# Kernel tuning notes

Measured on AMD Instinct MI355X. Metric: run time of the kernel, lower is better.

Reference implementation:

```python
import jax, jax.numpy as jnp
import numpy as np

B, T, E, H, R = 4, 256, 128, 8, 64
D = E // H


def _xavier(k, fan_in, fan_out, gain=1.0):
    a = gain * np.sqrt(6.0 / (fan_in + fan_out))
    return jax.random.uniform(k, (fan_in, fan_out), minval=-a, maxval=a, dtype=jnp.float32)


def setup_inputs() -> dict:
    key = jax.random.key(0)
    ks = jax.random.split(key, 16)
    g = 1.0 / np.sqrt(2.0)  # gain used for q/k/v when qkv_same_dim
    return {
        "query": jax.random.normal(ks[0], (B, T, E), jnp.float32),
        "velocity": jax.random.normal(ks[1], (B, T, 3, E), jnp.float32),
        "edge_feature": jax.random.normal(ks[2], (B, T, T, R), jnp.float32),
        "edge_direction": jax.random.normal(ks[3], (B, T, T, 3), jnp.float32),
        "cutoff": jax.random.uniform(ks[4], (B, T, T), jnp.float32),
        "Wq": _xavier(ks[5], E, E, g), "bq": jnp.zeros((E,), jnp.float32),
        "Wk": _xavier(ks[6], E, E, g), "bk": jnp.zeros((E,), jnp.float32),
        "Wv": _xavier(ks[7], E, 3 * E, g), "bv": jnp.zeros((3 * E,), jnp.float32),
        "Wo": _xavier(ks[8], E, 3 * E), "bo": jnp.zeros((3 * E,), jnp.float32),
        "Wvel": _xavier(ks[9], E, 3 * E), "bvel": jnp.zeros((3 * E,), jnp.float32),
        "Wdk": _xavier(ks[10], R, E), "bdk": jnp.zeros((E,), jnp.float32),
        "Wdv": _xavier(ks[11], R, 3 * E), "bdv": jnp.zeros((3 * E,), jnp.float32),
    }


def reference(query, velocity, edge_feature, edge_direction, cutoff,
              Wq, bq, Wk, bk, Wv, bv, Wo, bo, Wvel, bvel, Wdk, bdk, Wdv, bdv):
    b, t, e = query.shape
    h = H
    d = e // h
    scaling = d ** -0.5
    # projections
    q = ((query @ Wq + bq) * scaling).reshape(b, t, 1, h, d)   # [b,t,1,h,d]
    k = (query @ Wk + bk).reshape(b, 1, t, h, d)                # [b,1,t,h,d]
    v = (query @ Wv + bv).reshape(b, 1, t, h, 3 * d)            # [b,1,t,h,3d]
    # RBF distance gates (dense pairwise)
    dk = jax.nn.silu(edge_feature @ Wdk + bdk).reshape(b, t, t, h, d)
    dv = jax.nn.silu(edge_feature @ Wdv + bdv).reshape(b, t, t, h, 3 * d)
    v = v * dv                                                  # [b,t,t,h,3d]
    v, vp1, vp2 = jnp.split(v, 3, axis=-1)                      # each [b,t,t,h,d]
    # velocity channel
    velp = velocity @ Wvel + bvel                               # [b,t,3,3e]
    w1, w2, w3 = jnp.split(velp, 3, axis=-1)                    # each [b,t,3,e]
    velocity_dot = (w1 * w2).sum(axis=2)                        # [b,t,e]
    vel_r = velocity.reshape(b, t, 3, h, d)
    # elementwise (non-dot-product) attention weights
    aw = q * k * dk / np.float32(np.sqrt(d))                    # [b,t,t,h,d]
    awf = jnp.nan_to_num(jax.nn.softmax(aw, axis=2))
    c = cutoff[..., None, None]                                 # [b,t,t,1,1]
    attn = (awf * c * v * (c != 0)).sum(axis=2).reshape(b, t, e)
    o1, o2, o3 = jnp.split(attn @ Wo + bo, 3, axis=-1)          # each [b,t,e]
    # equivariant vector path
    vec1 = vel_r[:, None] * vp1[:, :, :, None]                  # [b,t,t,3,h,d]
    vec2 = vp2[:, :, :, None] * edge_direction[..., None, None]
    vec = ((vec1 + vec2).reshape(b, t, t, 3, e) * (c != 0)).sum(axis=2)  # [b,t,3,e]
    dx = velocity_dot * o2 + o3                                 # [b,t,e]
    dvec = w3 * o1[:, :, None, :] + vec                         # [b,t,3,e]
    return dx, dvec
```

## Files before the change

kernel.cpp:

```cpp
#include <hip/hip_runtime.h>
#include <hip/hip_bf16.h>
#include <math.h>

#define TT 256
#define EE 128
#define TJ 16
#define SRCB 28672
#define TSH 14336
#define GTB 16384
#define VTB 12288

typedef __attribute__((ext_vector_type(8))) short short8v;
typedef __attribute__((ext_vector_type(4))) short short4v;
typedef __attribute__((ext_vector_type(4))) float f32x4;

__device__ __forceinline__ float silu_f(float x) {
    return x * __builtin_amdgcn_rcpf(1.0f + __expf(-x));
}

__device__ __forceinline__ unsigned short f2bf(float f) {
    union { float f; unsigned u; } x; x.f = f;
    unsigned r = (x.u + 0x7FFFu + ((x.u >> 16) & 1u)) >> 16;
    return (unsigned short)r;
}

__device__ __forceinline__ unsigned cvt_pk_bf16(float lo, float hi) {
    unsigned r;
    asm("v_cvt_pk_bf16_f32 %0, %1, %2" : "=v"(r) : "v"(lo), "v"(hi));
    return r;
}

__device__ __forceinline__ float bflo(unsigned u) { return __uint_as_float(u << 16); }
__device__ __forceinline__ float bfhi(unsigned u) { return __uint_as_float(u & 0xffff0000u); }
__device__ __forceinline__ float bfu(unsigned short u) { return __uint_as_float(((unsigned)u) << 16); }

__global__ __launch_bounds__(256) void packW_kernel(
    const float* __restrict__ Wdk, const float* __restrict__ Wdv,
    unsigned short* __restrict__ wfrag) {
    const int idx = blockIdx.x * 256 + threadIdx.x;
    const int lane = idx & 63;
    const int kh = (idx >> 6) & 1;
    const int nn = (idx >> 7) & 7;
    const int w = idx >> 10;
    const float* Wsel; int wstride, colbase;
    if (w == 0) { Wsel = Wdk; wstride = 128; colbase = 0; }
    else { Wsel = Wdv; wstride = 384; colbase = (w - 1) * 128; }
    const int lrow = lane >> 4;
    const int lcol = lane & 15;
    const int col = colbase + nn * 16 + lcol;
    unsigned short* dst = wfrag + (size_t)idx * 8;
#pragma unroll
    for (int e = 0; e < 8; ++e) {
        const int k = kh * 32 + lrow * 8 + e;
        dst[e] = f2bf(Wsel[k * wstride + col]);
    }
}

__global__ __launch_bounds__(256) void phaseA_kernel(
    const float* __restrict__ query, const float* __restrict__ velocity,
    const float* __restrict__ Wq, const float* __restrict__ bq,
    const float* __restrict__ Wk, const float* __restrict__ bk,
    const float* __restrict__ Wv, const float* __restrict__ bv,
    const float* __restrict__ Wvel, const float* __restrict__ bvel,
    float* __restrict__ qs_ws, unsigned short* __restrict__ kkvvT,
    float* __restrict__ veldot_ws, float* __restrict__ w3_ws) {
    const int row = blockIdx.x;
    const int t = threadIdx.x;
    __shared__ float sIn[EE];
    __shared__ float sVel[3 * EE];
    __shared__ float sVelp[3 * 384];
    if (t < EE) sIn[t] = query[(size_t)row * EE + t];
    for (int idx = t; idx < 3 * EE; idx += 256)
        sVel[idx] = velocity[(size_t)row * 3 * EE + idx];
    __syncthreads();

    unsigned short* tb = kkvvT + (size_t)(row >> 4) * TSH;
    const int r16 = row & 15;
    for (int o = t; o < 640; o += 256) {
        if (o < 128) {
            int c = o;
            float acc = bq[c];
#pragma unroll 8
            for (int r = 0; r < 128; ++r) acc = fmaf(sIn[r], Wq[r * 128 + c], acc);
            qs_ws[(size_t)row * 128 + c] = acc * 0.25f;
        } else if (o < 256) {
            int c = o - 128;
            float acc = bk[c];
#pragma unroll 8
            for (int r = 0; r < 128; ++r) acc = fmaf(sIn[r], Wk[r * 128 + c], acc);
            const int sg = (r16 >> 2) ^ ((c >> 2) & 3);
            tb[c * 16 + sg * 4 + (r16 & 3)] = f2bf(acc);
        } else {
            int c = o - 256;
            float acc = bv[c];
#pragma unroll 8
            for (int r = 0; r < 128; ++r) acc = fmaf(sIn[r], Wv[r * 384 + c], acc);
            const int col = 128 + c;
            const int sg = (r16 >> 2) ^ ((col >> 2) & 3);
            tb[col * 16 + sg * 4 + (r16 & 3)] = f2bf(acc);
        }
    }
    for (int idx = t; idx < 384; idx += 256)
        tb[8192 + r16 * 384 + idx] = f2bf(sVel[idx]);

    for (int c = t; c < 384; c += 256) {
        float a0 = bvel[c], a1 = a0, a2 = a0;
#pragma unroll 8
        for (int r = 0; r < 128; ++r) {
            float w = Wvel[r * 384 + c];
            a0 = fmaf(sVel[r], w, a0);
            a1 = fmaf(sVel[128 + r], w, a1);
            a2 = fmaf(sVel[256 + r], w, a2);
        }
        sVelp[0 * 384 + c] = a0;
        sVelp[1 * 384 + c] = a1;
        sVelp[2 * 384 + c] = a2;
    }
    __syncthreads();
    if (t < 128) {
        int c = t;
        float vd = 0.f;
#pragma unroll
        for (int s = 0; s < 3; ++s)
            vd += sVelp[s * 384 + c] * sVelp[s * 384 + 128 + c];
        veldot_ws[(size_t)row * 128 + c] = vd;
#pragma unroll
        for (int s = 0; s < 3; ++s)
            w3_ws[((size_t)row * 3 + s) * 128 + c] = sVelp[s * 384 + 256 + c];
    }
}

__global__ __launch_bounds__(256, 3) void phaseB_kernel(
    const float* __restrict__ edge_feature, const float* __restrict__ edge_direction,
    const float* __restrict__ cutoff,
    const unsigned short* __restrict__ wfrag, const unsigned short* __restrict__ kkvvT,
    const float* __restrict__ bdk, const float* __restrict__ bdv,
    const float* __restrict__ qs_ws,
    float* __restrict__ attn_ws, float* __restrict__ vec_ws) {
    const int blk = blockIdx.x;
    const int x = blk & 7;
    const int slot = blk >> 3;
    const int b = x >> 1;
    const int i = ((x & 1) << 7) + slot;
    const int row = b * TT + i;

    const int t = threadIdx.x;
    const int wave = t >> 6;
    const int lane = t & 63;
    const int lrow = lane >> 4;
    const int lcol = lane & 15;

    __shared__ __align__(16) unsigned char smem[51712];
    unsigned char* sGates = smem;
    unsigned char* sVelB  = smem + 16384;
    unsigned char* sEFb   = smem + 28672;
    unsigned short* sKD   = (unsigned short*)(smem + 32768);
    unsigned short* sGV   = (unsigned short*)(smem + 37376);
    float* sCut           = (float*)(smem + 51200);
    float* sDirS          = (float*)(smem + 51328);
    float* sMrg           = (float*)smem;

    const float* Bsel;
    int colbase;
    if (wave == 0) { Bsel = bdk; colbase = 0; }
    else { Bsel = bdv; colbase = (wave - 1) * 128; }

    float biasv[8];
#pragma unroll
    for (int n = 0; n < 8; ++n)
        biasv[n] = Bsel[colbase + n * 16 + lcol];

    const unsigned short* wfbase = wfrag + ((size_t)wave * 1024 + lane) * 8;
    short8v bwr[16];
#pragma unroll
    for (int n = 0; n < 8; ++n) {
        bwr[2 * n]     = *(const short8v*)(wfbase + (size_t)n * 1024);
        bwr[2 * n + 1] = *(const short8v*)(wfbase + (size_t)n * 1024 + 512);
    }

    const int grp = t >> 7;
    const int c = t & 127;
    const float qsc = qs_ws[(size_t)row * 128 + c] * 0.25f * 1.44269504f;

    float l = 0.f, A = 0.f;
    float v0 = 0.f, v1 = 0.f, v2 = 0.f;

    const size_t ef_base = (size_t)row * TT * 64;
    const size_t cut_base = (size_t)row * TT;
    const size_t dir_base = (size_t)row * TT * 3;
    const unsigned char* kvT = (const unsigned char*)kkvvT + (size_t)(b * 16) * SRCB;

    const int ldsoff = (t & 192) * 16;
    const int gswz = (lrow ^ ((lcol >> 2) & 3)) * 4;

#pragma unroll
    for (int r = 0; r < 4; ++r)
        __builtin_amdgcn_global_load_lds(
            (const void*)(kvT + (size_t)r * 4096 + (size_t)t * 16),
            (void*)(sGates + r * 4096 + ldsoff), 16, 0, 0);
    {
        f32x4 e0 = ((const f32x4*)(edge_feature + ef_base))[t];
        const int erow = t >> 4;
        const int kq = t & 15;
        const unsigned plo = cvt_pk_bf16(e0[0], e0[1]);
        const unsigned phi = cvt_pk_bf16(e0[2], e0[3]);
        const int byteoff = (kq * 8) ^ ((erow & 7) << 4);
        *(int2*)(sEFb + erow * 128 + byteoff) = make_int2((int)plo, (int)phi);
        if (t < TJ) sCut[t] = cutoff[cut_base + t];
        if (t < TJ * 3) sDirS[t] = edge_direction[dir_base + t];
    }
    __syncthreads();

    f32x4 pEf;
    float pCut = 0.f, pDir = 0.f;
    int e = 0;
    for (int j0 = 0; j0 < TT; j0 += TJ) {
        {
            const unsigned char* src = kvT + (size_t)(j0 >> 4) * SRCB + GTB;
#pragma unroll
            for (int r = 0; r < 3; ++r)
                __builtin_amdgcn_global_load_lds(
                    (const void*)(src + (size_t)r * 4096 + (size_t)t * 16),
                    (void*)(sVelB + r * 4096 + ldsoff), 16, 0, 0);
        }
        {
            const int jn = (j0 + TJ) & 255;
            pEf = ((const f32x4*)(edge_feature + ef_base + (size_t)jn * 64))[t];
            pCut = (t < TJ) ? cutoff[cut_base + jn + t] : 0.f;
            pDir = (t < TJ * 3) ? edge_direction[dir_base + (size_t)jn * 3 + t] : 0.f;
        }
        {
            const unsigned short* gT = (const unsigned short*)sGates;
            const unsigned char* efb = sEFb + e * 2048;
            const int arow = lcol;
            const int swzb = (arow & 7) << 4;
            const short8v a0 = *(const short8v*)(efb + arow * 128 + ((lrow * 16) ^ swzb));
            const short8v a1 = *(const short8v*)(efb + arow * 128 + ((64 + lrow * 16) ^ swzb));

            short4v g4[8];
#pragma unroll
            for (int n = 0; n < 8; ++n)
                g4[n] = *(const short4v*)(gT + ((wave * 128 + n * 16 + lcol) * 16 + gswz));
#pragma unroll
            for (int n = 0; n < 8; ++n) {
                const int col = colbase + n * 16 + lcol;
                f32x4 acc = {biasv[n], biasv[n], biasv[n], biasv[n]};
                acc = __builtin_amdgcn_mfma_f32_16x16x32_bf16(a0, bwr[2 * n],     acc, 0, 0, 0);
                acc = __builtin_amdgcn_mfma_f32_16x16x32_bf16(a1, bwr[2 * n + 1], acc, 0, 0, 0);
                const float r0 = bfu((unsigned short)g4[n][0]) * silu_f(acc[0]);
                const float r1 = bfu((unsigned short)g4[n][1]) * silu_f(acc[1]);
                const float r2 = bfu((unsigned short)g4[n][2]) * silu_f(acc[2]);
                const float r3 = bfu((unsigned short)g4[n][3]) * silu_f(acc[3]);
                const unsigned w01 = cvt_pk_bf16(r0, r1);
                const unsigned w23 = cvt_pk_bf16(r2, r3);
                unsigned short* dst;
                if (wave == 0) {
                    dst = &sKD[col * 18 + lrow * 4];
                } else {
                    const int plane = (col >> 4) % 3;
                    const int cch = (col / 48) * 16 + lcol;
                    dst = &sGV[plane * 2304 + cch * 18 + lrow * 4];
                }
                *(unsigned*)(dst) = w01;
                *(unsigned*)(dst + 2) = w23;
            }
        }
        __syncthreads();

        if (j0 + TJ < TT) {
            const unsigned char* src = kvT + (size_t)((j0 >> 4) + 1) * SRCB;
#pragma unroll
            for (int r = 0; r < 4; ++r)
                __builtin_amdgcn_global_load_lds(
                    (const void*)(src + (size_t)r * 4096 + (size_t)t * 16),
                    (void*)(sGates + r * 4096 + ldsoff), 16, 0, 0);
        }
        {
            unsigned char* efb = sEFb + (e ^ 1) * 2048;
            const int erow = t >> 4;
            const int kq = t & 15;
            const unsigned plo = cvt_pk_bf16(pEf[0], pEf[1]);
            const unsigned phi = cvt_pk_bf16(pEf[2], pEf[3]);
            const int byteoff = (kq * 8) ^ ((erow & 7) << 4);
            *(int2*)(efb + erow * 128 + byteoff) = make_int2((int)plo, (int)phi);
            if (t < TJ) sCut[(e ^ 1) * TJ + t] = pCut;
            if (t < TJ * 3) sDirS[(e ^ 1) * TJ * 3 + t] = pDir;
        }
        {
            const unsigned short* svel = (const unsigned short*)sVelB;
            const float* cutE = sCut + e * TJ;
            const float* dirE = sDirS + e * TJ * 3;
            const int jlo = grp * (TJ / 2);
#pragma unroll
            for (int q = 0; q < 4; ++q) {
                const int jj = jlo + 2 * q;
                const unsigned kd2 = *(const unsigned*)(&sKD[c * 18 + jj]);
                const unsigned vg2 = *(const unsigned*)(&sGV[0 * 2304 + c * 18 + jj]);
                const unsigned p12 = *(const unsigned*)(&sGV[1 * 2304 + c * 18 + jj]);
                const unsigned p22 = *(const unsigned*)(&sGV[2 * 2304 + c * 18 + jj]);
                const float cut0 = cutE[jj];
                const float cut1 = cutE[jj + 1];
                const float p0 = exp2f(qsc * bflo(kd2));
                const float p1 = exp2f(qsc * bfhi(kd2));
                l += p0 + p1;
                A = fmaf(p0 * cut0, bflo(vg2), A);
                A = fmaf(p1 * cut1, bfhi(vg2), A);
                if (cut0 != 0.0f) {
                    const unsigned short* vp = svel + (size_t)jj * 384 + c;
                    const float w1 = bflo(p12), w2 = bflo(p22);
                    v0 = fmaf(bfu(vp[0]),   w1, fmaf(w2, dirE[jj * 3 + 0], v0));
                    v1 = fmaf(bfu(vp[128]), w1, fmaf(w2, dirE[jj * 3 + 1], v1));
                    v2 = fmaf(bfu(vp[256]), w1, fmaf(w2, dirE[jj * 3 + 2], v2));
                }
                if (cut1 != 0.0f) {
                    const unsigned short* vp = svel + (size_t)(jj + 1) * 384 + c;
                    const float w1 = bfhi(p12), w2 = bfhi(p22);
                    v0 = fmaf(bfu(vp[0]),   w1, fmaf(w2, dirE[jj * 3 + 3], v0));
                    v1 = fmaf(bfu(vp[128]), w1, fmaf(w2, dirE[jj * 3 + 4], v1));
                    v2 = fmaf(bfu(vp[256]), w1, fmaf(w2, dirE[jj * 3 + 5], v2));
                }
            }
        }
        __syncthreads();
        e ^= 1;
    }

    if (grp == 1) {
        sMrg[c * 5 + 0] = l;  sMrg[c * 5 + 1] = A;
        sMrg[c * 5 + 2] = v0; sMrg[c * 5 + 3] = v1; sMrg[c * 5 + 4] = v2;
    }
    __syncthreads();
    if (grp == 0) {
        const float L = l + sMrg[c * 5 + 0];
        const float Aa = A + sMrg[c * 5 + 1];
        const float attn = (L > 0.f) ? (Aa * __builtin_amdgcn_rcpf(L)) : 0.f;
        attn_ws[(size_t)row * 128 + c] = attn;
        vec_ws[((size_t)row * 3 + 0) * 128 + c] = v0 + sMrg[c * 5 + 2];
        vec_ws[((size_t)row * 3 + 1) * 128 + c] = v1 + sMrg[c * 5 + 3];
        vec_ws[((size_t)row * 3 + 2) * 128 + c] = v2 + sMrg[c * 5 + 4];
    }
}

__global__ __launch_bounds__(256) void phaseC_kernel(
    const float* __restrict__ Wo, const float* __restrict__ bo,
    const float* __restrict__ attn_ws, const float* __restrict__ veldot_ws,
    const float* __restrict__ w3_ws, const float* __restrict__ vec_ws,
    float* __restrict__ out) {
    const int row = blockIdx.x;
    const int t = threadIdx.x;
    __shared__ float sAttn[128];
    __shared__ float sO[384];
    if (t < 128) sAttn[t] = attn_ws[(size_t)row * 128 + t];
    __syncthreads();
    for (int o = t; o < 384; o += 256) {
        float acc = bo[o];
#pragma unroll 8
        for (int r = 0; r < 128; ++r) acc = fmaf(sAttn[r], Wo[r * 384 + o], acc);
        sO[o] = acc;
    }
    __syncthreads();
    if (t < 128) {
        int c = t;
        float o1 = sO[c], o2 = sO[128 + c], o3 = sO[256 + c];
        float dx = fmaf(veldot_ws[(size_t)row * 128 + c], o2, o3);
        out[(size_t)row * 128 + c] = dx;
#pragma unroll
        for (int s = 0; s < 3; ++s) {
            size_t idx = ((size_t)row * 3 + s) * 128 + c;
            out[131072 + idx] = fmaf(w3_ws[idx], o1, vec_ws[idx]);
        }
    }
}

extern "C" void kernel_launch(void* const* d_in, const int* in_sizes, int n_in,
                              void* d_out, int out_size, void* d_ws, size_t ws_size,
                              hipStream_t stream) {
    (void)in_sizes; (void)n_in; (void)out_size; (void)ws_size;
    const float* query          = (const float*)d_in[0];
    const float* velocity       = (const float*)d_in[1];
    const float* edge_feature   = (const float*)d_in[2];
    const float* edge_direction = (const float*)d_in[3];
    const float* cutoff         = (const float*)d_in[4];
    const float* Wq   = (const float*)d_in[5];  const float* bq   = (const float*)d_in[6];
    const float* Wk   = (const float*)d_in[7];  const float* bk   = (const float*)d_in[8];
    const float* Wv   = (const float*)d_in[9];  const float* bv   = (const float*)d_in[10];
    const float* Wo   = (const float*)d_in[11]; const float* bo   = (const float*)d_in[12];
    const float* Wvel = (const float*)d_in[13]; const float* bvel = (const float*)d_in[14];
    const float* Wdk  = (const float*)d_in[15]; const float* bdk  = (const float*)d_in[16];
    const float* Wdv  = (const float*)d_in[17]; const float* bdv  = (const float*)d_in[18];

    float* ws        = (float*)d_ws;
    float* qs_ws     = ws;
    float* veldot_ws = ws + 131072;
    float* w3_ws     = ws + 262144;
    float* attn_ws   = ws + 655360;
    float* vec_ws    = ws + 786432;
    unsigned short* wfrag = (unsigned short*)(ws + 1179648);
    unsigned short* kkvvT = (unsigned short*)(ws + 1196032);

    float* out = (float*)d_out;

    hipLaunchKernelGGL(packW_kernel, dim3(16), dim3(256), 0, stream,
        Wdk, Wdv, wfrag);
    hipLaunchKernelGGL(phaseA_kernel, dim3(1024), dim3(256), 0, stream,
        query, velocity, Wq, bq, Wk, bk, Wv, bv, Wvel, bvel,
        qs_ws, kkvvT, veldot_ws, w3_ws);
    hipLaunchKernelGGL(phaseB_kernel, dim3(1024), dim3(256), 0, stream,
        edge_feature, edge_direction, cutoff,
        wfrag, kkvvT, bdk, bdv, qs_ws, attn_ws, vec_ws);
    hipLaunchKernelGGL(phaseC_kernel, dim3(1024), dim3(256), 0, stream,
        Wo, bo, attn_ws, veldot_ws, w3_ws, vec_ws, out);
}
```

Baseline: 150.7 us.

## Prefetch gate tiles into registers instead of LDS and unroll loop by two

The kk/vv gate fragments used by each MFMA output are no longer staged through shared memory with global_load_lds. Each lane now loads them straight from global memory into registers, one tile ahead, using a ping-pong register pair (gA/gB). The j-loop is unrolled by two through a templated tile body, so the edge-feature double-buffer index becomes a compile-time constant. This cuts LDS use from about 51.7KB to 35.3KB, which could allow more resident blocks, at the cost of extra VGPRs and uncoalesced short4 global loads whose latency must be hidden by the prefetch.

```diff
diff --git a/kernel.cpp b/kernel.cpp
--- a/kernel.cpp
+++ b/kernel.cpp
@@ -130,6 +130,122 @@
     }
 }
 
+template <int E>
+__device__ __forceinline__ void tile_body(
+    int j0,
+    const float* __restrict__ edge_feature, const float* __restrict__ cutoff,
+    const float* __restrict__ edge_direction,
+    size_t ef_base, size_t cut_base, size_t dir_base,
+    const unsigned char* kvT,
+    unsigned char* sVelB, unsigned char* sEFb,
+    unsigned short* sKD, unsigned short* sGV, float* sCut, float* sDirS,
+    int t, int wave, int lrow, int lcol, int ldsoff, int gswz,
+    int colbase, const float (&biasv)[8], const short8v (&bwr)[16],
+    short4v (&gcur)[8], short4v (&gnext)[8],
+    f32x4& pEf, float& pCut, float& pDir,
+    int grp, int c, float qsc,
+    float& l, float& A, float& v0, float& v1, float& v2) {
+
+    {
+        const unsigned char* src = kvT + (size_t)(j0 >> 4) * SRCB + GTB;
+#pragma unroll
+        for (int r = 0; r < 3; ++r)
+            __builtin_amdgcn_global_load_lds(
+                (const void*)(src + (size_t)r * 4096 + (size_t)t * 16),
+                (void*)(sVelB + r * 4096 + ldsoff), 16, 0, 0);
+    }
+    {
+        const int jn = (j0 + TJ) & 255;
+        pEf = ((const f32x4*)(edge_feature + ef_base + (size_t)jn * 64))[t];
+        pCut = (t < TJ) ? cutoff[cut_base + jn + t] : 0.f;
+        pDir = (t < TJ * 3) ? edge_direction[dir_base + (size_t)jn * 3 + t] : 0.f;
+    }
+    if (j0 + TJ < TT) {
+        const unsigned short* gsrc = (const unsigned short*)(kvT + (size_t)((j0 >> 4) + 1) * SRCB);
+#pragma unroll
+        for (int n = 0; n < 8; ++n)
+            gnext[n] = *(const short4v*)(gsrc + ((wave * 128 + n * 16 + lcol) * 16 + gswz));
+    }
+    {
+        const unsigned char* efb = sEFb + E * 2048;
+        const int swzb = (lcol & 7) << 4;
+        const short8v a0 = *(const short8v*)(efb + lcol * 128 + ((lrow * 16) ^ swzb));
+        const short8v a1 = *(const short8v*)(efb + lcol * 128 + ((64 + lrow * 16) ^ swzb));
+#pragma unroll
+        for (int n = 0; n < 8; ++n) {
+            const int col = colbase + n * 16 + lcol;
+            f32x4 acc = {biasv[n], biasv[n], biasv[n], biasv[n]};
+            acc = __builtin_amdgcn_mfma_f32_16x16x32_bf16(a0, bwr[2 * n],     acc, 0, 0, 0);
+            acc = __builtin_amdgcn_mfma_f32_16x16x32_bf16(a1, bwr[2 * n + 1], acc, 0, 0, 0);
+            const float r0 = bfu((unsigned short)gcur[n][0]) * silu_f(acc[0]);
+            const float r1 = bfu((unsigned short)gcur[n][1]) * silu_f(acc[1]);
+            const float r2 = bfu((unsigned short)gcur[n][2]) * silu_f(acc[2]);
+            const float r3 = bfu((unsigned short)gcur[n][3]) * silu_f(acc[3]);
+            const unsigned w01 = cvt_pk_bf16(r0, r1);
+            const unsigned w23 = cvt_pk_bf16(r2, r3);
+            unsigned short* dst;
+            if (wave == 0) {
+                dst = &sKD[col * 18 + lrow * 4];
+            } else {
+                const int plane = (col >> 4) % 3;
+                const int cch = (col / 48) * 16 + lcol;
+                dst = &sGV[plane * 2304 + cch * 18 + lrow * 4];
+            }
+            *(unsigned*)(dst) = w01;
+            *(unsigned*)(dst + 2) = w23;
+        }
+    }
+    __syncthreads();
+
+    {
+        unsigned char* efb = sEFb + (E ^ 1) * 2048;
+        const int erow = t >> 4;
+        const int kq = t & 15;
+        const unsigned plo = cvt_pk_bf16(pEf[0], pEf[1]);
+        const unsigned phi = cvt_pk_bf16(pEf[2], pEf[3]);
+        const int byteoff = (kq * 8) ^ ((erow & 7) << 4);
+        *(int2*)(efb + erow * 128 + byteoff) = make_int2((int)plo, (int)phi);
+        if (t < TJ) sCut[(E ^ 1) * TJ + t] = pCut;
+        if (t < TJ * 3) sDirS[(E ^ 1) * TJ * 3 + t] = pDir;
+    }
+    {
+        const unsigned short* svel = (const unsigned short*)sVelB;
+        const float* cutE = sCut + E * TJ;
+        const float* dirE = sDirS + E * TJ * 3;
+        const int jlo = grp * (TJ / 2);
+#pragma unroll
+        for (int q = 0; q < 4; ++q) {
+            const int jj = jlo + 2 * q;
+            const unsigned kd2 = *(const unsigned*)(&sKD[c * 18 + jj]);
+            const unsigned vg2 = *(const unsigned*)(&sGV[0 * 2304 + c * 18 + jj]);
+            const unsigned p12 = *(const unsigned*)(&sGV[1 * 2304 + c * 18 + jj]);
+            const unsigned p22 = *(const unsigned*)(&sGV[2 * 2304 + c * 18 + jj]);
+            const float cut0 = cutE[jj];
+            const float cut1 = cutE[jj + 1];
+            const float p0 = exp2f(qsc * bflo(kd2));
+            const float p1 = exp2f(qsc * bfhi(kd2));
+            l += p0 + p1;
+            A = fmaf(p0 * cut0, bflo(vg2), A);
+            A = fmaf(p1 * cut1, bfhi(vg2), A);
+            if (cut0 != 0.0f) {
+                const unsigned short* vp = svel + (size_t)jj * 384 + c;
+                const float w1 = bflo(p12), w2 = bflo(p22);
+                v0 = fmaf(bfu(vp[0]),   w1, fmaf(w2, dirE[jj * 3 + 0], v0));
+                v1 = fmaf(bfu(vp[128]), w1, fmaf(w2, dirE[jj * 3 + 1], v1));
+                v2 = fmaf(bfu(vp[256]), w1, fmaf(w2, dirE[jj * 3 + 2], v2));
+            }
+            if (cut1 != 0.0f) {
+                const unsigned short* vp = svel + (size_t)(jj + 1) * 384 + c;
+                const float w1 = bfhi(p12), w2 = bfhi(p22);
+                v0 = fmaf(bfu(vp[0]),   w1, fmaf(w2, dirE[jj * 3 + 3], v0));
+                v1 = fmaf(bfu(vp[128]), w1, fmaf(w2, dirE[jj * 3 + 4], v1));
+                v2 = fmaf(bfu(vp[256]), w1, fmaf(w2, dirE[jj * 3 + 5], v2));
+            }
+        }
+    }
+    __syncthreads();
+}
+
 __global__ __launch_bounds__(256, 3) void phaseB_kernel(
     const float* __restrict__ edge_feature, const float* __restrict__ edge_direction,
     const float* __restrict__ cutoff,
@@ -150,14 +266,13 @@
     const int lrow = lane >> 4;
     const int lcol = lane & 15;
 
-    __shared__ __align__(16) unsigned char smem[51712];
-    unsigned char* sGates = smem;
-    unsigned char* sVelB  = smem + 16384;
-    unsigned char* sEFb   = smem + 28672;
-    unsigned short* sKD   = (unsigned short*)(smem + 32768);
-    unsigned short* sGV   = (unsigned short*)(smem + 37376);
-    float* sCut           = (float*)(smem + 51200);
-    float* sDirS          = (float*)(smem + 51328);
+    __shared__ __align__(16) unsigned char smem[35328];
+    unsigned char* sVelB  = smem;
+    unsigned char* sEFb   = smem + 12288;
+    unsigned short* sKD   = (unsigned short*)(smem + 16384);
+    unsigned short* sGV   = (unsigned short*)(smem + 20992);
+    float* sCut           = (float*)(smem + 34816);
+    float* sDirS          = (float*)(smem + 34944);
     float* sMrg           = (float*)smem;
 
     const float* Bsel;
@@ -193,11 +308,13 @@
     const int ldsoff = (t & 192) * 16;
     const int gswz = (lrow ^ ((lcol >> 2) & 3)) * 4;
 
-#pragma unroll
-    for (int r = 0; r < 4; ++r)
-        __builtin_amdgcn_global_load_lds(
-            (const void*)(kvT + (size_t)r * 4096 + (size_t)t * 16),
-            (void*)(sGates + r * 4096 + ldsoff), 16, 0, 0);
+    short4v gA[8], gB[8];
+    {
+        const unsigned short* gsrc = (const unsigned short*)kvT;
+#pragma unroll
+        for (int n = 0; n < 8; ++n)
+            gA[n] = *(const short4v*)(gsrc + ((wave * 128 + n * 16 + lcol) * 16 + gswz));
+    }
     {
         f32x4 e0 = ((const f32x4*)(edge_feature + ef_base))[t];
         const int erow = t >> 4;
@@ -213,116 +330,19 @@
 
     f32x4 pEf;
     float pCut = 0.f, pDir = 0.f;
-    int e = 0;
-    for (int j0 = 0; j0 < TT; j0 += TJ) {
-        {
-            const unsigned char* src = kvT + (size_t)(j0 >> 4) * SRCB + GTB;
-#pragma unroll
-            for (int r = 0; r < 3; ++r)
-                __builtin_amdgcn_global_load_lds(
-                    (const void*)(src + (size_t)r * 4096 + (size_t)t * 16),
-                    (void*)(sVelB + r * 4096 + ldsoff), 16, 0, 0);
-        }
-        {
-            const int jn = (j0 + TJ) & 255;
-            pEf = ((const f32x4*)(edge_feature + ef_base + (size_t)jn * 64))[t];
-            pCut = (t < TJ) ? cutoff[cut_base + jn + t] : 0.f;
-            pDir = (t < TJ * 3) ? edge_direction[dir_base + (size_t)jn * 3 + t] : 0.f;
-        }
-        {
-            const unsigned short* gT = (const unsigned short*)sGates;
-            const unsigned char* efb = sEFb + e * 2048;
-            const int arow = lcol;
-            const int swzb = (arow & 7) << 4;
-            const short8v a0 = *(const short8v*)(efb + arow * 128 + ((lrow * 16) ^ swzb));
-            const short8v a1 = *(const short8v*)(efb + arow * 128 + ((64 + lrow * 16) ^ swzb));
-
-            short4v g4[8];
-#pragma unroll
-            for (int n = 0; n < 8; ++n)
-                g4[n] = *(const short4v*)(gT + ((wave * 128 + n * 16 + lcol) * 16 + gswz));
-#pragma unroll
-            for (int n = 0; n < 8; ++n) {
-                const int col = colbase + n * 16 + lcol;
-                f32x4 acc = {biasv[n], biasv[n], biasv[n], biasv[n]};
-                acc = __builtin_amdgcn_mfma_f32_16x16x32_bf16(a0, bwr[2 * n],     acc, 0, 0, 0);
-                acc = __builtin_amdgcn_mfma_f32_16x16x32_bf16(a1, bwr[2 * n + 1], acc, 0, 0, 0);
-                const float r0 = bfu((unsigned short)g4[n][0]) * silu_f(acc[0]);
-                const float r1 = bfu((unsigned short)g4[n][1]) * silu_f(acc[1]);
-                const float r2 = bfu((unsigned short)g4[n][2]) * silu_f(acc[2]);
-                const float r3 = bfu((unsigned short)g4[n][3]) * silu_f(acc[3]);
-                const unsigned w01 = cvt_pk_bf16(r0, r1);
-                const unsigned w23 = cvt_pk_bf16(r2, r3);
-                unsigned short* dst;
-                if (wave == 0) {
-                    dst = &sKD[col * 18 + lrow * 4];
-                } else {
-                    const int plane = (col >> 4) % 3;
-                    const int cch = (col / 48) * 16 + lcol;
-                    dst = &sGV[plane * 2304 + cch * 18 + lrow * 4];
-                }
-                *(unsigned*)(dst) = w01;
-                *(unsigned*)(dst + 2) = w23;
-            }
-        }
-        __syncthreads();
-
-        if (j0 + TJ < TT) {
-            const unsigned char* src = kvT + (size_t)((j0 >> 4) + 1) * SRCB;
-#pragma unroll
-            for (int r = 0; r < 4; ++r)
-                __builtin_amdgcn_global_load_lds(
-                    (const void*)(src + (size_t)r * 4096 + (size_t)t * 16),
-                    (void*)(sGates + r * 4096 + ldsoff), 16, 0, 0);
-        }
-        {
-            unsigned char* efb = sEFb + (e ^ 1) * 2048;
-            const int erow = t >> 4;
-            const int kq = t & 15;
-            const unsigned plo = cvt_pk_bf16(pEf[0], pEf[1]);
-            const unsigned phi = cvt_pk_bf16(pEf[2], pEf[3]);
-            const int byteoff = (kq * 8) ^ ((erow & 7) << 4);
-            *(int2*)(efb + erow * 128 + byteoff) = make_int2((int)plo, (int)phi);
-            if (t < TJ) sCut[(e ^ 1) * TJ + t] = pCut;
-            if (t < TJ * 3) sDirS[(e ^ 1) * TJ * 3 + t] = pDir;
-        }
-        {
-            const unsigned short* svel = (const unsigned short*)sVelB;
-            const float* cutE = sCut + e * TJ;
-            const float* dirE = sDirS + e * TJ * 3;
-            const int jlo = grp * (TJ / 2);
-#pragma unroll
-            for (int q = 0; q < 4; ++q) {
-                const int jj = jlo + 2 * q;
-                const unsigned kd2 = *(const unsigned*)(&sKD[c * 18 + jj]);
-                const unsigned vg2 = *(const unsigned*)(&sGV[0 * 2304 + c * 18 + jj]);
-                const unsigned p12 = *(const unsigned*)(&sGV[1 * 2304 + c * 18 + jj]);
-                const unsigned p22 = *(const unsigned*)(&sGV[2 * 2304 + c * 18 + jj]);
-                const float cut0 = cutE[jj];
-                const float cut1 = cutE[jj + 1];
-                const float p0 = exp2f(qsc * bflo(kd2));
-                const float p1 = exp2f(qsc * bfhi(kd2));
-                l += p0 + p1;
-                A = fmaf(p0 * cut0, bflo(vg2), A);
-                A = fmaf(p1 * cut1, bfhi(vg2), A);
-                if (cut0 != 0.0f) {
-                    const unsigned short* vp = svel + (size_t)jj * 384 + c;
-                    const float w1 = bflo(p12), w2 = bflo(p22);
-                    v0 = fmaf(bfu(vp[0]),   w1, fmaf(w2, dirE[jj * 3 + 0], v0));
-                    v1 = fmaf(bfu(vp[128]), w1, fmaf(w2, dirE[jj * 3 + 1], v1));
-                    v2 = fmaf(bfu(vp[256]), w1, fmaf(w2, dirE[jj * 3 + 2], v2));
-                }
-                if (cut1 != 0.0f) {
-                    const unsigned short* vp = svel + (size_t)(jj + 1) * 384 + c;
-                    const float w1 = bfhi(p12), w2 = bfhi(p22);
-                    v0 = fmaf(bfu(vp[0]),   w1, fmaf(w2, dirE[jj * 3 + 3], v0));
-                    v1 = fmaf(bfu(vp[128]), w1, fmaf(w2, dirE[jj * 3 + 4], v1));
-                    v2 = fmaf(bfu(vp[256]), w1, fmaf(w2, dirE[jj * 3 + 5], v2));
-                }
-            }
-        }
-        __syncthreads();
-        e ^= 1;
+    for (int jt = 0; jt < TT; jt += 2 * TJ) {
+        tile_body<0>(jt, edge_feature, cutoff, edge_direction,
+                     ef_base, cut_base, dir_base, kvT,
+                     sVelB, sEFb, sKD, sGV, sCut, sDirS,
+                     t, wave, lrow, lcol, ldsoff, gswz,
+                     colbase, biasv, bwr, gA, gB, pEf, pCut, pDir,
+                     grp, c, qsc, l, A, v0, v1, v2);
+        tile_body<1>(jt + TJ, edge_feature, cutoff, edge_direction,
+                     ef_base, cut_base, dir_base, kvT,
+                     sVelB, sEFb, sKD, sGV, sCut, sDirS,
+                     t, wave, lrow, lcol, ldsoff, gswz,
+                     colbase, biasv, bwr, gB, gA, pEf, pCut, pDir,
+                     grp, c, qsc, l, A, v0, v1, v2);
     }
 
     if (grp == 1) {
```

Result: slower. 244.8 us (+62.4%).
